# Kernel optimization log

Measured on AMD Instinct MI355X. Metric: run time of the kernel, lower is better.

## Reference

```python
import jax, jax.numpy as jnp
import numpy as np

D_MODEL = 1024
N_HEADS = 16
N_KV = 4
HEAD_DIM = 64
R = 256
B, N = 2, 2048


def setup_inputs() -> dict:
    key = jax.random.key(0)
    ks = jax.random.split(key, 5)
    x = jax.random.normal(ks[0], (B, N, D_MODEL), jnp.float32)
    # rotary cos/sin table: (N, HEAD_DIM//2, 2)
    inv = 1.0 / (10000.0 ** (jnp.arange(0, HEAD_DIM, 2, dtype=jnp.float32) / HEAD_DIM))
    ang = jnp.arange(N, dtype=jnp.float32)[:, None] * inv[None, :]
    freqs_cis = jnp.stack([jnp.cos(ang), jnp.sin(ang)], axis=-1)
    s = 0.02
    Wq = jax.random.normal(ks[1], (D_MODEL, N_HEADS * HEAD_DIM), jnp.float32) * s
    Wk = jax.random.normal(ks[2], (D_MODEL, N_KV * HEAD_DIM), jnp.float32) * s
    Wv = jax.random.normal(ks[3], (D_MODEL, N_KV * HEAD_DIM), jnp.float32) * s
    Wo = jax.random.normal(ks[4], (N_HEADS * HEAD_DIM, D_MODEL), jnp.float32) * s
    return dict(x=x, freqs_cis=freqs_cis, Wq=Wq, Wk=Wk, Wv=Wv, Wo=Wo)


def _select_pairs(scores_i, best_b_i, r):
    """Greedy top-r pair selection with unique-b constraint (one batch row)."""
    half = scores_i.shape[0]
    order = jnp.argsort(-scores_i)  # descending by best similarity

    def step(carry, a_local):
        used, count = carry
        b_local = best_b_i[a_local]
        take = jnp.logical_and(jnp.logical_not(used[b_local]), count < r)
        used = used.at[b_local].set(used[b_local] | take)
        count = count + take.astype(jnp.int32)
        return (used, count), (take, a_local.astype(jnp.int32), b_local.astype(jnp.int32))

    (_, count), (takes, a_locs, b_locs) = jax.lax.scan(
        step, (jnp.zeros(half, bool), jnp.int32(0)), order)
    pos = jnp.cumsum(takes.astype(jnp.int32)) - 1
    idx = jnp.where(takes, pos, r)  # dump non-taken into slot r
    sel_a = jnp.zeros(r + 1, jnp.int32).at[idx].set(a_locs)[:r]
    sel_b = jnp.zeros(r + 1, jnp.int32).at[idx].set(b_locs)[:r]
    valid = jnp.arange(r) < count  # pad (if fewer than r unique) with first pair
    sel_a = jnp.where(valid, sel_a, sel_a[0])
    sel_b = jnp.where(valid, sel_b, sel_b[0])
    return sel_a, sel_b


def bipartite_indices(metric, r):
    """Returns (global_a, global_b, keep_idx) for merge/unmerge."""
    Bm, Nm, _ = metric.shape
    a = metric[:, 0::2]  # (B, half, C)
    b = metric[:, 1::2]
    an = a / jnp.maximum(jnp.linalg.norm(a, axis=-1, keepdims=True), 1e-12)
    bn = b / jnp.maximum(jnp.linalg.norm(b, axis=-1, keepdims=True), 1e-12)
    scores = jnp.einsum('bic,bjc->bij', an, bn)  # (B, half, half)
    best_scores = scores.max(axis=2)
    best_b = scores.argmax(axis=2)
    sel_a, sel_b = jax.vmap(lambda s, m: _select_pairs(s, m, r))(best_scores, best_b)
    global_a = 2 * sel_a      # even indices
    global_b = 2 * sel_b + 1  # odd indices
    bidx = jnp.arange(Bm)[:, None]
    keep_mask = jnp.ones((Bm, Nm), bool).at[bidx, global_b].set(False)
    # stable argsort puts kept (False) positions first, in original order
    keep_idx = jnp.argsort(~keep_mask, axis=1)[:, :Nm - r]
    return global_a, global_b, keep_idx


def merge(x, global_a, global_b, keep_idx):
    Bm = x.shape[0]
    bidx = jnp.arange(Bm)[:, None]
    xa = jnp.take_along_axis(x, global_a[..., None], axis=1)
    xb = jnp.take_along_axis(x, global_b[..., None], axis=1)
    x_out = x.at[bidx, global_a].set((xa + xb) * 0.5)
    return jnp.take_along_axis(x_out, keep_idx[..., None], axis=1)


def unmerge(xm, global_a, global_b, keep_idx, n_orig):
    Bm, _, C = xm.shape
    bidx = jnp.arange(Bm)[:, None]
    out = jnp.zeros((Bm, n_orig, C), xm.dtype).at[bidx, keep_idx].set(xm)
    xa = jnp.take_along_axis(out, global_a[..., None], axis=1)
    return out.at[bidx, global_b].set(xa)


def _rope(t, freqs):
    # t: (B, N, H, HD), freqs: (N, HD//2, 2)
    cos = freqs[None, :, None, :, 0]
    sin = freqs[None, :, None, :, 1]
    t1 = t[..., 0::2]
    t2 = t[..., 1::2]
    rot = jnp.stack([t1 * cos - t2 * sin, t1 * sin + t2 * cos], axis=-1)
    return rot.reshape(t.shape)


def _attention(x_m, freqs, Wq, Wk, Wv, Wo):
    Bm, Nm, _ = x_m.shape
    q = (x_m @ Wq).reshape(Bm, Nm, N_HEADS, HEAD_DIM)
    k = (x_m @ Wk).reshape(Bm, Nm, N_KV, HEAD_DIM)
    v = (x_m @ Wv).reshape(Bm, Nm, N_KV, HEAD_DIM)
    q = _rope(q, freqs)
    k = _rope(k, freqs)
    rep = N_HEADS // N_KV
    k = jnp.repeat(k, rep, axis=2)
    v = jnp.repeat(v, rep, axis=2)
    att = jnp.einsum('bqhd,bkhd->bhqk', q, k) / np.sqrt(HEAD_DIM).astype(np.float32)
    w = jax.nn.softmax(att, axis=-1)
    o = jnp.einsum('bhqk,bkhd->bqhd', w, v).reshape(Bm, Nm, N_HEADS * HEAD_DIM)
    return o @ Wo


def reference(x, freqs_cis, Wq, Wk, Wv, Wo):
    n = x.shape[1]
    metric = jax.lax.stop_gradient(x @ Wk)  # k_proj under no_grad
    ga, gb, ki = bipartite_indices(metric, R)
    x_m = merge(x, ga, gb, ki)
    n_merged = x_m.shape[1]
    out_m = _attention(x_m, freqs_cis[:n_merged], Wq, Wk, Wv, Wo)
    return unmerge(out_m, ga, gb, ki, n)
```

## Files before the change

### kernel.cpp

```cpp
#include <hip/hip_runtime.h>
#include <hip/hip_bf16.h>
#include <math.h>

#define BB 2
#define NN 2048
#define DM 1024
#define NH 16
#define NKV 4
#define HD 64
#define RR 256
#define HALF 1024
#define NM 1792
#define NT 28
#define NSPL 4

typedef __bf16 bf16x8 __attribute__((ext_vector_type(8)));
typedef float f32x4 __attribute__((ext_vector_type(4)));

__device__ inline unsigned pk2(float a, float b) {
  union { __bf16 h; unsigned short u; } ua, ub;
  ua.h = (__bf16)a;
  ub.h = (__bf16)b;
  return (unsigned)ua.u | ((unsigned)ub.u << 16);
}

__device__ inline unsigned shu(unsigned v, int s) {
  return (unsigned)__shfl((int)v, s, 64);
}

__device__ __forceinline__ void async16(const void* g, void* l) {
  __builtin_amdgcn_global_load_lds(
      (const __attribute__((address_space(1))) void*)g,
      (__attribute__((address_space(3))) void*)l, 16, 0, 0);
}

__global__ __launch_bounds__(256) void gemm_bf16(
    const __bf16* __restrict__ A, const __bf16* __restrict__ Bt,
    float* __restrict__ C, int M, int N, int K) {
  __shared__ __align__(16) __bf16 As[8192];
  __shared__ __align__(16) __bf16 Bs[4096];
  const int bm0 = blockIdx.x * 128;
  const int bn0 = blockIdx.y * 64;
  const int w = threadIdx.x >> 6;
  const int lane = threadIdx.x & 63;
  f32x4 acc[2][4];
#pragma unroll
  for (int i = 0; i < 2; ++i)
#pragma unroll
    for (int nt = 0; nt < 4; ++nt) acc[i][nt] = (f32x4){0.f, 0.f, 0.f, 0.f};
  for (int kk = 0; kk < K; kk += 64) {
    __syncthreads();
#pragma unroll
    for (int it = 0; it < 4; ++it) {
      const int c = it * 256 + w * 64 + lane;
      async16(A + (size_t)(bm0 + ((c >> 7) << 4) + (c & 15)) * K + kk +
                  (((c >> 6) & 1) << 5) + (((c >> 4) & 3) << 3),
              &As[(it * 256 + w * 64) * 8]);
    }
#pragma unroll
    for (int it = 0; it < 2; ++it) {
      const int c = it * 256 + w * 64 + lane;
      async16(Bt + (size_t)(bn0 + ((c >> 7) << 4) + (c & 15)) * K + kk +
                  (((c >> 6) & 1) << 5) + (((c >> 4) & 3) << 3),
              &Bs[(it * 256 + w * 64) * 8]);
    }
    __syncthreads();
#pragma unroll
    for (int s = 0; s < 2; ++s) {
      bf16x8 a0 = *(const bf16x8*)&As[((2 * w) * 128 + s * 64 + lane) * 8];
      bf16x8 a1 = *(const bf16x8*)&As[((2 * w + 1) * 128 + s * 64 + lane) * 8];
#pragma unroll
      for (int nt = 0; nt < 4; ++nt) {
        bf16x8 bfr = *(const bf16x8*)&Bs[(nt * 128 + s * 64 + lane) * 8];
        acc[0][nt] =
            __builtin_amdgcn_mfma_f32_16x16x32_bf16(a0, bfr, acc[0][nt], 0, 0, 0);
        acc[1][nt] =
            __builtin_amdgcn_mfma_f32_16x16x32_bf16(a1, bfr, acc[1][nt], 0, 0, 0);
      }
    }
  }
  const int g = lane >> 4, ml = lane & 15;
#pragma unroll
  for (int i = 0; i < 2; ++i)
#pragma unroll
    for (int nt = 0; nt < 4; ++nt)
#pragma unroll
      for (int r = 0; r < 4; ++r)
        C[(size_t)(bm0 + (2 * w + i) * 16 + g * 4 + r) * N + bn0 + nt * 16 +
          ml] = acc[i][nt][r];
}

__global__ __launch_bounds__(256) void gemm_wo(
    const __bf16* __restrict__ A, const __bf16* __restrict__ Bt,
    const int* __restrict__ keep_idx, const int* __restrict__ dst2,
    float* __restrict__ out, int M, int N, int K) {
  __shared__ __align__(16) __bf16 As[8192];
  __shared__ __align__(16) __bf16 Bs[4096];
  const int bm0 = blockIdx.x * 128;
  const int bn0 = blockIdx.y * 64;
  const int w = threadIdx.x >> 6;
  const int lane = threadIdx.x & 63;
  f32x4 acc[2][4];
#pragma unroll
  for (int i = 0; i < 2; ++i)
#pragma unroll
    for (int nt = 0; nt < 4; ++nt) acc[i][nt] = (f32x4){0.f, 0.f, 0.f, 0.f};
  for (int kk = 0; kk < K; kk += 64) {
    __syncthreads();
#pragma unroll
    for (int it = 0; it < 4; ++it) {
      const int c = it * 256 + w * 64 + lane;
      async16(A + (size_t)(bm0 + ((c >> 7) << 4) + (c & 15)) * K + kk +
                  (((c >> 6) & 1) << 5) + (((c >> 4) & 3) << 3),
              &As[(it * 256 + w * 64) * 8]);
    }
#pragma unroll
    for (int it = 0; it < 2; ++it) {
      const int c = it * 256 + w * 64 + lane;
      async16(Bt + (size_t)(bn0 + ((c >> 7) << 4) + (c & 15)) * K + kk +
                  (((c >> 6) & 1) << 5) + (((c >> 4) & 3) << 3),
              &Bs[(it * 256 + w * 64) * 8]);
    }
    __syncthreads();
#pragma unroll
    for (int s = 0; s < 2; ++s) {
      bf16x8 a0 = *(const bf16x8*)&As[((2 * w) * 128 + s * 64 + lane) * 8];
      bf16x8 a1 = *(const bf16x8*)&As[((2 * w + 1) * 128 + s * 64 + lane) * 8];
#pragma unroll
      for (int nt = 0; nt < 4; ++nt) {
        bf16x8 bfr = *(const bf16x8*)&Bs[(nt * 128 + s * 64 + lane) * 8];
        acc[0][nt] =
            __builtin_amdgcn_mfma_f32_16x16x32_bf16(a0, bfr, acc[0][nt], 0, 0, 0);
        acc[1][nt] =
            __builtin_amdgcn_mfma_f32_16x16x32_bf16(a1, bfr, acc[1][nt], 0, 0, 0);
      }
    }
  }
  const int g = lane >> 4, ml = lane & 15;
#pragma unroll
  for (int i = 0; i < 2; ++i)
#pragma unroll
    for (int r = 0; r < 4; ++r) {
      const int row = bm0 + (2 * w + i) * 16 + g * 4 + r;
      const int bb = row / NM, tt = row % NM;
      const int p1 = keep_idx[bb * NM + tt];
      const int p2 = dst2[bb * NM + tt];
#pragma unroll
      for (int nt = 0; nt < 4; ++nt) {
        const int col = bn0 + nt * 16 + ml;
        float v = acc[i][nt][r];
        out[((size_t)(bb * NN + p1)) * DM + col] = v;
        if (p2 >= 0) out[((size_t)(bb * NN + p2)) * DM + col] = v;
      }
    }
}

__global__ __launch_bounds__(256) void gemm3t(
    const __bf16* __restrict__ Ah, const __bf16* __restrict__ Al,
    const __bf16* __restrict__ Bh, const __bf16* __restrict__ Bl,
    float* __restrict__ C0, float* __restrict__ C1, int M, int N, int K) {
  __shared__ __align__(16) __bf16 Ahs[4096], Als[4096], Bhs[4096], Bls[4096];
  const int z = blockIdx.z;
  float* C = z ? C1 : C0;
  const int kof = z * (K / 2);
  const int bm0 = blockIdx.x * 64;
  const int bn0 = blockIdx.y * 64;
  const int w = threadIdx.x >> 6;
  const int lane = threadIdx.x & 63;
  f32x4 acc[4];
#pragma unroll
  for (int nt = 0; nt < 4; ++nt) acc[nt] = (f32x4){0.f, 0.f, 0.f, 0.f};
  for (int kk = kof; kk < kof + K / 2; kk += 64) {
    __syncthreads();
#pragma unroll
    for (int it = 0; it < 2; ++it) {
      const int c = it * 256 + w * 64 + lane;
      const size_t ra = (size_t)(bm0 + ((c >> 7) << 4) + (c & 15)) * K;
      const size_t rb = (size_t)(bn0 + ((c >> 7) << 4) + (c & 15)) * K;
      const int col = kk + (((c >> 6) & 1) << 5) + (((c >> 4) & 3) << 3);
      const int lb = (it * 256 + w * 64) * 8;
      async16(Ah + ra + col, &Ahs[lb]);
      async16(Al + ra + col, &Als[lb]);
      async16(Bh + rb + col, &Bhs[lb]);
      async16(Bl + rb + col, &Bls[lb]);
    }
    __syncthreads();
#pragma unroll
    for (int s = 0; s < 2; ++s) {
      bf16x8 ah = *(const bf16x8*)&Ahs[((w * 2 + s) * 64 + lane) * 8];
      bf16x8 al = *(const bf16x8*)&Als[((w * 2 + s) * 64 + lane) * 8];
#pragma unroll
      for (int nt = 0; nt < 4; ++nt) {
        bf16x8 bh = *(const bf16x8*)&Bhs[((nt * 2 + s) * 64 + lane) * 8];
        bf16x8 bl = *(const bf16x8*)&Bls[((nt * 2 + s) * 64 + lane) * 8];
        acc[nt] = __builtin_amdgcn_mfma_f32_16x16x32_bf16(al, bh, acc[nt], 0, 0, 0);
        acc[nt] = __builtin_amdgcn_mfma_f32_16x16x32_bf16(ah, bl, acc[nt], 0, 0, 0);
        acc[nt] = __builtin_amdgcn_mfma_f32_16x16x32_bf16(ah, bh, acc[nt], 0, 0, 0);
      }
    }
  }
  const int g = lane >> 4, ml = lane & 15;
#pragma unroll
  for (int nt = 0; nt < 4; ++nt)
#pragma unroll
    for (int r = 0; r < 4; ++r)
      C[(size_t)(bm0 + w * 16 + g * 4 + r) * N + bn0 + nt * 16 + ml] =
          acc[nt][r];
}

__global__ __launch_bounds__(256) void gemm_scam(
    const __bf16* __restrict__ Ah, const __bf16* __restrict__ Al,
    const __bf16* __restrict__ Bh, const __bf16* __restrict__ Bl,
    float* __restrict__ sval, int* __restrict__ sidx) {
  __shared__ __align__(16) __bf16 Ahs[4096], Als[4096], Bhs[4096], Bls[4096];
  const size_t zo = (size_t)blockIdx.z * HALF * 256;
  const int bm0 = blockIdx.x * 64;
  const int bn0 = blockIdx.y * 64;
  const int w = threadIdx.x >> 6;
  const int lane = threadIdx.x & 63;
  f32x4 acc[4];
#pragma unroll
  for (int nt = 0; nt < 4; ++nt) acc[nt] = (f32x4){0.f, 0.f, 0.f, 0.f};
  for (int kk = 0; kk < 256; kk += 64) {
    __syncthreads();
#pragma unroll
    for (int it = 0; it < 2; ++it) {
      const int c = it * 256 + w * 64 + lane;
      const size_t ra = zo + (size_t)(bm0 + ((c >> 7) << 4) + (c & 15)) * 256;
      const size_t rb = zo + (size_t)(bn0 + ((c >> 7) << 4) + (c & 15)) * 256;
      const int col = kk + (((c >> 6) & 1) << 5) + (((c >> 4) & 3) << 3);
      const int lb = (it * 256 + w * 64) * 8;
      async16(Ah + ra + col, &Ahs[lb]);
      async16(Al + ra + col, &Als[lb]);
      async16(Bh + rb + col, &Bhs[lb]);
      async16(Bl + rb + col, &Bls[lb]);
    }
    __syncthreads();
#pragma unroll
    for (int s = 0; s < 2; ++s) {
      bf16x8 ah = *(const bf16x8*)&Ahs[((w * 2 + s) * 64 + lane) * 8];
      bf16x8 al = *(const bf16x8*)&Als[((w * 2 + s) * 64 + lane) * 8];
#pragma unroll
      for (int nt = 0; nt < 4; ++nt) {
        bf16x8 bh = *(const bf16x8*)&Bhs[((nt * 2 + s) * 64 + lane) * 8];
        bf16x8 bl = *(const bf16x8*)&Bls[((nt * 2 + s) * 64 + lane) * 8];
        acc[nt] = __builtin_amdgcn_mfma_f32_16x16x32_bf16(al, bh, acc[nt], 0, 0, 0);
        acc[nt] = __builtin_amdgcn_mfma_f32_16x16x32_bf16(ah, bl, acc[nt], 0, 0, 0);
        acc[nt] = __builtin_amdgcn_mfma_f32_16x16x32_bf16(ah, bh, acc[nt], 0, 0, 0);
      }
    }
  }
  const int g = lane >> 4, ml = lane & 15;
#pragma unroll
  for (int r = 0; r < 4; ++r) {
    float bv = acc[0][r];
    int bc = bn0 + ml;
#pragma unroll
    for (int nt = 1; nt < 4; ++nt) {
      float v = acc[nt][r];
      int c = bn0 + nt * 16 + ml;
      if (v > bv) { bv = v; bc = c; }
    }
#pragma unroll
    for (int off = 1; off < 16; off <<= 1) {
      float vo = __shfl_xor(bv, off, 64);
      int co = __shfl_xor(bc, off, 64);
      if (vo > bv || (vo == bv && co < bc)) { bv = vo; bc = co; }
    }
    if (ml == 0) {
      const int row = bm0 + w * 16 + g * 4 + r;
      const size_t o = ((size_t)blockIdx.z * HALF + row) * 16 + (bn0 >> 6);
      sval[o] = bv;
      sidx[o] = bc;
    }
  }
}

__global__ __launch_bounds__(256) void prep_in(
    const float* __restrict__ Wq, const float* __restrict__ Wk,
    const float* __restrict__ Wv, const float* __restrict__ Wo,
    const float* __restrict__ x, __bf16* __restrict__ Wqkvt,
    __bf16* __restrict__ Wktl, __bf16* __restrict__ Wot,
    __bf16* __restrict__ xh, __bf16* __restrict__ xl) {
  const int z = blockIdx.x;
  if (z >= 640) {
    const int i = (z - 640) * 256 + threadIdx.x;
    float4 v = ((const float4*)x)[i];
    float f[4] = {v.x, v.y, v.z, v.w};
    union { __bf16 h[4]; uint2 u; } H, L;
#pragma unroll
    for (int j = 0; j < 4; ++j) {
      __bf16 hh = (__bf16)f[j];
      H.h[j] = hh;
      L.h[j] = (__bf16)(f[j] - (float)hh);
    }
    ((uint2*)xh)[i] = H.u;
    ((uint2*)xl)[i] = L.u;
    return;
  }
  __shared__ float ld[64][65];
  const float* src;
  __bf16* dsth;
  __bf16* dstl = nullptr;
  int N, k0, n0, rowoff;
  if (z < 256) {
    src = Wq; N = 1024; k0 = (z >> 4) << 6; n0 = (z & 15) << 6;
    dsth = Wqkvt; rowoff = 0;
  } else if (z < 320) {
    int zz = z - 256;
    src = Wk; N = 256; k0 = (zz >> 2) << 6; n0 = (zz & 3) << 6;
    dsth = Wqkvt; rowoff = 1024; dstl = Wktl;
  } else if (z < 384) {
    int zz = z - 320;
    src = Wv; N = 256; k0 = (zz >> 2) << 6; n0 = (zz & 3) << 6;
    dsth = Wqkvt; rowoff = 1280;
  } else {
    int zz = z - 384;
    src = Wo; N = 1024; k0 = (zz >> 4) << 6; n0 = (zz & 15) << 6;
    dsth = Wot; rowoff = 0;
  }
  for (int i = threadIdx.x; i < 1024; i += 256) {
    int r = i >> 4, c4 = i & 15;
    float4 v = *(const float4*)(src + (size_t)(k0 + r) * N + n0 + c4 * 4);
    ld[r][c4 * 4 + 0] = v.x;
    ld[r][c4 * 4 + 1] = v.y;
    ld[r][c4 * 4 + 2] = v.z;
    ld[r][c4 * 4 + 3] = v.w;
  }
  __syncthreads();
  for (int i = threadIdx.x; i < 4096; i += 256) {
    int n = i >> 6, k = i & 63;
    float v = ld[k][n];
    __bf16 hh = (__bf16)v;
    dsth[(size_t)(rowoff + n0 + n) * 1024 + k0 + k] = hh;
    if (dstl)
      dstl[(size_t)(n0 + n) * 1024 + k0 + k] = (__bf16)(v - (float)hh);
  }
}

__global__ __launch_bounds__(256) void normalize_split(
    const float* __restrict__ m0, const float* __restrict__ m1,
    __bf16* __restrict__ anh, __bf16* __restrict__ anl,
    __bf16* __restrict__ bnh, __bf16* __restrict__ bnl) {
  const int row = blockIdx.x;
  const int b = row >> 11;
  const int r = row & 2047;
  const int t = threadIdx.x;
  float v = m0[(size_t)row * 256 + t] + m1[(size_t)row * 256 + t];
  float ss = v * v;
#pragma unroll
  for (int o = 32; o > 0; o >>= 1) ss += __shfl_xor(ss, o, 64);
  __shared__ float wsum[4];
  if ((t & 63) == 0) wsum[t >> 6] = ss;
  __syncthreads();
  float tot = wsum[0] + wsum[1] + wsum[2] + wsum[3];
  float inv = 1.f / fmaxf(sqrtf(tot), 1e-12f);
  float nv = v * inv;
  __bf16 hh = (__bf16)nv;
  __bf16 ll = (__bf16)(nv - (float)hh);
  size_t o = ((size_t)b * HALF + (r >> 1)) * 256 + t;
  if (r & 1) {
    bnh[o] = hh;
    bnl[o] = ll;
  } else {
    anh[o] = hh;
    anl[o] = ll;
  }
}

__global__ __launch_bounds__(512) void sort_desc(
    const float* __restrict__ sval, const int* __restrict__ sidx,
    int* __restrict__ best_b, int* __restrict__ order) {
  const int b = blockIdx.x;
  __shared__ float sv[1024];
  __shared__ int si[1024];
  for (int i = threadIdx.x; i < 1024; i += 512) {
    const size_t base = ((size_t)b * HALF + i) * 16;
    float bv = sval[base];
    int bc = sidx[base];
#pragma unroll
    for (int e = 1; e < 16; ++e) {
      float v = sval[base + e];
      int c = sidx[base + e];
      if (v > bv || (v == bv && c < bc)) { bv = v; bc = c; }
    }
    sv[i] = bv;
    si[i] = i;
    best_b[b * HALF + i] = bc;
  }
  __syncthreads();
  for (int k = 2; k <= 1024; k <<= 1) {
    for (int j = k >> 1; j > 0; j >>= 1) {
      for (int t = threadIdx.x; t < 1024; t += 512) {
        int ixj = t ^ j;
        if (ixj > t) {
          bool dir = ((t & k) == 0);
          float va = sv[t], vb = sv[ixj];
          int ia = si[t], ib = si[ixj];
          bool before = (vb > va) || (vb == va && ib < ia);
          if (before == dir) {
            sv[t] = vb; sv[ixj] = va;
            si[t] = ib; si[ixj] = ia;
          }
        }
      }
      __syncthreads();
    }
  }
  for (int i = threadIdx.x; i < 1024; i += 512) order[b * HALF + i] = si[i];
}

__global__ __launch_bounds__(256) void select_and_index(
    const int* __restrict__ best_b, const int* __restrict__ order,
    int* __restrict__ keep_idx, int* __restrict__ partner,
    int* __restrict__ dst2) {
  const int b = blockIdx.x;
  __shared__ int rankA[HALF];
  __shared__ int minrank[HALF];
  __shared__ int taken[HALF];
  __shared__ int sel_a[RR], sel_b[RR];
  __shared__ int removed[NN];
  __shared__ int src_row[NN];
  __shared__ int tsum[256];
  const int t = threadIdx.x;

  for (int i = t; i < HALF; i += 256) { minrank[i] = 0x7fffffff; taken[i] = 0; }
  for (int i = t; i < NN; i += 256) {
    removed[i] = 0;
    partner[b * NN + i] = -1;
  }
  for (int i = t; i < NM; i += 256) dst2[b * NM + i] = -1;
  __syncthreads();
  int ord[4];
#pragma unroll
  for (int q = 0; q < 4; ++q) {
    int step = t * 4 + q;
    ord[q] = order[b * HALF + step];
    rankA[ord[q]] = step;
  }
  __syncthreads();
#pragma unroll
  for (int q = 0; q < 4; ++q) {
    int a = t * 4 + q;
    atomicMin(&minrank[best_b[b * HALF + a]], rankA[a]);
  }
  __syncthreads();
  for (int i = t; i < HALF; i += 256) {
    int mr = minrank[i];
    if (mr != 0x7fffffff) taken[mr] = 1;
  }
  __syncthreads();
  int c[4];
  int mysum = 0;
#pragma unroll
  for (int q = 0; q < 4; ++q) { c[q] = taken[t * 4 + q]; mysum += c[q]; }
  tsum[t] = mysum;
  __syncthreads();
  for (int off = 1; off < 256; off <<= 1) {
    int v = (t >= off) ? tsum[t - off] : 0;
    __syncthreads();
    tsum[t] += v;
    __syncthreads();
  }
  int run = tsum[t] - mysum;
#pragma unroll
  for (int q = 0; q < 4; ++q) {
    if (c[q] && run < RR) {
      int a = ord[q];
      sel_a[run] = 2 * a;
      sel_b[run] = 2 * best_b[b * HALF + a] + 1;
    }
    run += c[q];
  }
  __syncthreads();
  const int cnt = min(tsum[255], RR);
  if (t >= cnt) { sel_a[t] = sel_a[0]; sel_b[t] = sel_b[0]; }
  __syncthreads();
  {
    int ga = sel_a[t], gb = sel_b[t];
    removed[gb] = 1;
    partner[b * NN + ga] = gb;
  }
  __syncthreads();
  int myc = 0;
#pragma unroll
  for (int q = 0; q < 8; ++q) myc += !removed[8 * t + q];
  tsum[t] = myc;
  __syncthreads();
  for (int off = 1; off < 256; off <<= 1) {
    int v = (t >= off) ? tsum[t - off] : 0;
    __syncthreads();
    tsum[t] += v;
    __syncthreads();
  }
  int pos = tsum[t] - myc;
#pragma unroll
  for (int q = 0; q < 8; ++q) {
    int p = 8 * t + q;
    int sr = -1;
    if (!removed[p]) {
      if (pos < NM) {
        keep_idx[b * NM + pos] = p;
        sr = pos;
      }
      ++pos;
    }
    src_row[p] = sr;
  }
  __syncthreads();
  {
    int sr = src_row[sel_a[t]];
    dst2[b * NM + sr] = sel_b[t];
  }
}

__global__ __launch_bounds__(256) void merge_kernel(
    const float* __restrict__ x, const int* __restrict__ keep_idx,
    const int* __restrict__ partner, __bf16* __restrict__ x_mb) {
  const int mrow = blockIdx.x;
  const int b = mrow / NM;
  const int t = mrow % NM;
  const int p = keep_idx[b * NM + t];
  const int pp = partner[b * NN + p];
  const float4* src =
      reinterpret_cast<const float4*>(x + ((size_t)b * NN + p) * DM);
  float4 val = src[threadIdx.x];
  if (pp >= 0) {
    const float4* s2 =
        reinterpret_cast<const float4*>(x + ((size_t)b * NN + pp) * DM);
    float4 v2 = s2[threadIdx.x];
    val.x = 0.5f * (val.x + v2.x);
    val.y = 0.5f * (val.y + v2.y);
    val.z = 0.5f * (val.z + v2.z);
    val.w = 0.5f * (val.w + v2.w);
  }
  union { __bf16 h[4]; uint2 u; } U;
  U.h[0] = (__bf16)val.x;
  U.h[1] = (__bf16)val.y;
  U.h[2] = (__bf16)val.z;
  U.h[3] = (__bf16)val.w;
  ((uint2*)(x_mb + (size_t)mrow * DM))[threadIdx.x] = U.u;
}

__global__ __launch_bounds__(256) void prep_qkv(
    const float* __restrict__ qkv, const float* __restrict__ fc,
    __bf16* __restrict__ qbh, __bf16* __restrict__ kbh,
    __bf16* __restrict__ vtb) {
  __shared__ float ld[64][65];
  const int z = blockIdx.x;
  if (z < BB * NM) {
    const int row = z;
    const int t = row % NM;
    const int b = row / NM;
    for (int idx = threadIdx.x; idx < 640; idx += 256) {
      int u = idx & 31;
      float c = fc[(t * 32 + u) * 2];
      float s = fc[(t * 32 + u) * 2 + 1];
      if (idx < 512) {
        int h = idx >> 5;
        const float* p = qkv + (size_t)row * 1536 + h * 64 + 2 * u;
        float x1 = p[0], x2 = p[1];
        __bf16* d = qbh + ((size_t)(b * NH + h) * NM + t) * 64 + 2 * u;
        d[0] = (__bf16)((x1 * c - x2 * s) * 0.125f);
        d[1] = (__bf16)((x1 * s + x2 * c) * 0.125f);
      } else {
        int h = (idx - 512) >> 5;
        const float* p = qkv + (size_t)row * 1536 + 1024 + h * 64 + 2 * u;
        float x1 = p[0], x2 = p[1];
        __bf16* d = kbh + ((size_t)(b * NKV + h) * NM + t) * 64 + 2 * u;
        d[0] = (__bf16)(x1 * c - x2 * s);
        d[1] = (__bf16)(x1 * s + x2 * c);
      }
    }
    return;
  }
  int bid = z - BB * NM;
  const int kt = bid % (NM / 64); bid /= (NM / 64);
  const int kvh = bid % NKV;
  const int b = bid / NKV;
  const int j0 = kt * 64;
  for (int t2 = threadIdx.x; t2 < 1024; t2 += 256) {
    int key = t2 >> 4, c4 = t2 & 15;
    float4 v4 = *reinterpret_cast<const float4*>(
        qkv + (size_t)(b * NM + j0 + key) * 1536 + 1280 + kvh * 64 + c4 * 4);
    ld[key][c4 * 4 + 0] = v4.x;
    ld[key][c4 * 4 + 1] = v4.y;
    ld[key][c4 * 4 + 2] = v4.z;
    ld[key][c4 * 4 + 3] = v4.w;
  }
  __syncthreads();
  const int dim = threadIdx.x >> 2, kc = threadIdx.x & 3;
  __bf16* out = vtb + ((size_t)(b * NKV + kvh) * 64 + dim) * NM + j0 + kc * 16;
#pragma unroll
  for (int kk = 0; kk < 16; ++kk) out[kk] = (__bf16)ld[kc * 16 + kk][dim];
}

__global__ __launch_bounds__(512) void attn_mfma(
    const __bf16* __restrict__ qbh, const __bf16* __restrict__ kbh,
    const __bf16* __restrict__ vtb, float* __restrict__ pl,
    __bf16* __restrict__ pacc) {
  __shared__ __align__(16) __bf16 Ks[2][4096];
  __shared__ __align__(16) __bf16 Vs[2][4096];
  int bid = blockIdx.x;
  const int qt2 = bid % (NM / 32); bid /= (NM / 32);
  const int split = bid % NSPL; bid /= NSPL;
  const int kvh = bid % NKV;
  const int b = bid / NKV;
  const int w = threadIdx.x >> 6;
  const int lane = threadIdx.x & 63;
  const int h = kvh * 4 + (w & 3);
  const int qt = qt2 * 32 + (w >> 2) * 16;
  const int g = lane >> 4;
  const int ml = lane & 15;

  const __bf16* qrow = qbh + ((size_t)(b * NH + h) * NM + qt + ml) * 64;
  bf16x8 qa0 = *reinterpret_cast<const bf16x8*>(qrow + g * 8);
  bf16x8 qa1 = *reinterpret_cast<const bf16x8*>(qrow + 32 + g * 8);

  f32x4 acc[4];
#pragma unroll
  for (int mt = 0; mt < 4; ++mt) acc[mt] = (f32x4){0.f, 0.f, 0.f, 0.f};
  float lsum = 0.f;

  const __bf16* kp = kbh + (size_t)(b * NKV + kvh) * NM * 64;
  const __bf16* vp = vtb + (size_t)(b * NKV + kvh) * 64 * NM;
  const int src0 = ((lane >> 4) & 1) * 32 + ml;
  const int src1 = src0 + 16;
  const int sel = g >> 1;
  const int c = threadIdx.x;
  const int lb = w * 512;
  const size_t koff = (size_t)(((c >> 7) << 4) + (c & 15)) * 64 +
                      (((c >> 6) & 1) << 5) + (((c >> 4) & 3) << 3);
  const size_t voff = (size_t)(((c >> 7) << 4) + (c & 15)) * NM +
                      (((c >> 6) & 1) << 5) + (((c >> 4) & 3) << 3);

  const int jt0 = split * (NT / NSPL);
  const int niter = NT / NSPL;
  async16(kp + (size_t)jt0 * 64 * 64 + koff, &Ks[0][lb]);
  async16(vp + jt0 * 64 + voff, &Vs[0][lb]);

  for (int i = 0; i < niter; ++i) {
    __syncthreads();
    if (i + 1 < niter) {
      const int jn = jt0 + i + 1;
      async16(kp + (size_t)jn * 64 * 64 + koff, &Ks[(i + 1) & 1][lb]);
      async16(vp + jn * 64 + voff, &Vs[(i + 1) & 1][lb]);
    }
    const __bf16* Kb = Ks[i & 1];
    const __bf16* Vb = Vs[i & 1];
    f32x4 S[4];
#pragma unroll
    for (int nt = 0; nt < 4; ++nt) {
      bf16x8 k0 = *(const bf16x8*)&Kb[(nt * 128 + lane) * 8];
      bf16x8 k1 = *(const bf16x8*)&Kb[(nt * 128 + 64 + lane) * 8];
      f32x4 s4 = (f32x4){0.f, 0.f, 0.f, 0.f};
      s4 = __builtin_amdgcn_mfma_f32_16x16x32_bf16(k0, qa0, s4, 0, 0, 0);
      s4 = __builtin_amdgcn_mfma_f32_16x16x32_bf16(k1, qa1, s4, 0, 0, 0);
      S[nt] = s4;
    }
    float p[4][4];
#pragma unroll
    for (int nt = 0; nt < 4; ++nt)
#pragma unroll
      for (int r = 0; r < 4; ++r) {
        p[nt][r] = __expf(S[nt][r]);
        lsum += p[nt][r];
      }
    unsigned pk[4][2];
#pragma unroll
    for (int nt = 0; nt < 4; ++nt) {
      pk[nt][0] = pk2(p[nt][0], p[nt][1]);
      pk[nt][1] = pk2(p[nt][2], p[nt][3]);
    }
    unsigned A00 = shu(pk[0][0], src0), A01 = shu(pk[0][1], src0);
    unsigned A10 = shu(pk[1][0], src0), A11 = shu(pk[1][1], src0);
    unsigned B00 = shu(pk[0][0], src1), B01 = shu(pk[0][1], src1);
    unsigned B10 = shu(pk[1][0], src1), B11 = shu(pk[1][1], src1);
    unsigned C00 = shu(pk[2][0], src0), C01 = shu(pk[2][1], src0);
    unsigned C10 = shu(pk[3][0], src0), C11 = shu(pk[3][1], src0);
    unsigned D00 = shu(pk[2][0], src1), D01 = shu(pk[2][1], src1);
    unsigned D10 = shu(pk[3][0], src1), D11 = shu(pk[3][1], src1);
    union { uint4 u; bf16x8 v; } P0, P1;
    P0.u.x = sel ? A10 : A00; P0.u.y = sel ? A11 : A01;
    P0.u.z = sel ? B10 : B00; P0.u.w = sel ? B11 : B01;
    P1.u.x = sel ? C10 : C00; P1.u.y = sel ? C11 : C01;
    P1.u.z = sel ? D10 : D00; P1.u.w = sel ? D11 : D01;
#pragma unroll
    for (int mt = 0; mt < 4; ++mt) {
      bf16x8 v0 = *(const bf16x8*)&Vb[(mt * 128 + lane) * 8];
      bf16x8 v1 = *(const bf16x8*)&Vb[(mt * 128 + 64 + lane) * 8];
      acc[mt] = __builtin_amdgcn_mfma_f32_16x16x32_bf16(v0, P0.v, acc[mt], 0, 0, 0);
      acc[mt] = __builtin_amdgcn_mfma_f32_16x16x32_bf16(v1, P1.v, acc[mt], 0, 0, 0);
    }
  }
  lsum += __shfl_xor(lsum, 16, 64);
  lsum += __shfl_xor(lsum, 32, 64);
  const size_t row = (size_t)(b * NH + h) * NM + qt + ml;
  if (g == 0) pl[row * NSPL + split] = lsum;
  __bf16* pa = pacc + (row * NSPL + split) * 64;
#pragma unroll
  for (int mt = 0; mt < 4; ++mt) {
    uint2 u;
    u.x = pk2(acc[mt][0], acc[mt][1]);
    u.y = pk2(acc[mt][2], acc[mt][3]);
    *reinterpret_cast<uint2*>(pa + mt * 16 + g * 4) = u;
  }
}

__global__ __launch_bounds__(256) void attn_combine(
    const float* __restrict__ pl, const __bf16* __restrict__ pacc,
    __bf16* __restrict__ attn_ob) {
  const size_t rid = (size_t)blockIdx.x * 4 + (threadIdx.x >> 6);
  const int d = threadIdx.x & 63;
  float num = 0.f, den = 0.f;
#pragma unroll
  for (int s = 0; s < NSPL; ++s) {
    num += (float)pacc[(rid * NSPL + s) * 64 + d];
    den += pl[rid * NSPL + s];
  }
  float o = num / den;
  const int q = (int)(rid % NM);
  const int h = (int)((rid / NM) % NH);
  const int b = (int)(rid / ((size_t)NM * NH));
  attn_ob[((size_t)(b * NM + q)) * DM + h * 64 + d] = (__bf16)o;
}

extern "C" void kernel_launch(void* const* d_in, const int* in_sizes, int n_in,
                              void* d_out, int out_size, void* d_ws,
                              size_t ws_size, hipStream_t stream) {
  const float* x = (const float*)d_in[0];
  const float* fc = (const float*)d_in[1];
  const float* Wq = (const float*)d_in[2];
  const float* Wk = (const float*)d_in[3];
  const float* Wv = (const float*)d_in[4];
  const float* Wo = (const float*)d_in[5];
  float* out = (float*)d_out;

  char* ws = (char*)d_ws;
  size_t off = 0;
  auto alloc = [&](size_t bytes) {
    void* p = ws + off;
    off += (bytes + 255) & ~(size_t)255;
    return p;
  };
  float* metric0 = (float*)alloc((size_t)BB * NN * 256 * 4);
  float* metric1 = (float*)alloc((size_t)BB * NN * 256 * 4);
  int* best_b = (int*)alloc((size_t)BB * HALF * 4);
  int* order = (int*)alloc((size_t)BB * HALF * 4);
  int* keep_idx = (int*)alloc((size_t)BB * NM * 4);
  int* partner = (int*)alloc((size_t)BB * NN * 4);
  int* dst2 = (int*)alloc((size_t)BB * NM * 4);
  float* sval = (float*)alloc((size_t)BB * HALF * 16 * 4);
  int* sidx = (int*)alloc((size_t)BB * HALF * 16 * 4);
  char* bigreg = (char*)alloc((size_t)30 * 1024 * 1024);
  __bf16* xh = (__bf16*)bigreg;
  __bf16* xl = (__bf16*)(bigreg + (size_t)8704 * 1024);
  __bf16* anh = (__bf16*)bigreg;
  __bf16* anl = (__bf16*)(bigreg + (size_t)1100 * 1024);
  __bf16* bnh = (__bf16*)(bigreg + (size_t)2200 * 1024);
  __bf16* bnl = (__bf16*)(bigreg + (size_t)3300 * 1024);
  float* qkv = (float*)bigreg;
  __bf16* pacc = (__bf16*)bigreg;
  __bf16* x_mb = (__bf16*)alloc((size_t)BB * NM * DM * 2);
  __bf16* qbh = (__bf16*)alloc((size_t)BB * NH * NM * 64 * 2);
  __bf16* kbh = (__bf16*)alloc((size_t)BB * NKV * NM * 64 * 2);
  __bf16* vtb = (__bf16*)alloc((size_t)BB * NKV * 64 * NM * 2);
  __bf16* attn_ob = (__bf16*)alloc((size_t)BB * NM * DM * 2);
  float* pl = (float*)alloc((size_t)BB * NH * NM * NSPL * 4);
  __bf16* Wqkvt = (__bf16*)alloc((size_t)1536 * DM * 2);
  __bf16* Wktl = (__bf16*)alloc((size_t)256 * DM * 2);
  __bf16* Wot = (__bf16*)alloc((size_t)DM * DM * 2);
  const __bf16* Wkth = Wqkvt + (size_t)1024 * 1024;

  prep_in<<<640 + (BB * NN * DM / 4) / 256, 256, 0, stream>>>(
      Wq, Wk, Wv, Wo, x, Wqkvt, Wktl, Wot, xh, xl);
  gemm3t<<<dim3(64, 4, 2), 256, 0, stream>>>(xh, xl, Wkth, Wktl, metric0,
                                             metric1, BB * NN, 256, DM);
  normalize_split<<<BB * NN, 256, 0, stream>>>(metric0, metric1, anh, anl, bnh,
                                               bnl);
  gemm_scam<<<dim3(16, 16, 2), 256, 0, stream>>>(anh, anl, bnh, bnl, sval,
                                                 sidx);
  sort_desc<<<BB, 512, 0, stream>>>(sval, sidx, best_b, order);
  select_and_index<<<BB, 256, 0, stream>>>(best_b, order, keep_idx, partner,
                                           dst2);
  merge_kernel<<<BB * NM, 256, 0, stream>>>(x, keep_idx, partner, x_mb);
  gemm_bf16<<<dim3(28, 24), 256, 0, stream>>>(x_mb, Wqkvt, qkv, BB * NM, 1536,
                                              DM);
  prep_qkv<<<BB * NM + BB * NKV * (NM / 64), 256, 0, stream>>>(qkv, fc, qbh,
                                                               kbh, vtb);
  attn_mfma<<<BB * NKV * NSPL * (NM / 32), 512, 0, stream>>>(qbh, kbh, vtb, pl,
                                                             pacc);
  attn_combine<<<(BB * NH * NM) / 4, 256, 0, stream>>>(pl, pacc, attn_ob);
  gemm_wo<<<dim3(28, 16), 256, 0, stream>>>(attn_ob, Wot, keep_idx, dst2, out,
                                            BB * NM, DM, DM);
}
```

Measured before the change: 291.6 us.

## Shrink attention blocks to 256 threads and drop K/V double buffering

The attention kernel now uses 4 waves per block, each covering one head of the KV group for a 16-row query tile, instead of 8 waves covering two query tiles. The double-buffered async K/V prefetch is replaced by a single buffer that is loaded and then synchronised before use every iteration. This halves shared memory per block and doubles the block count, aiming for higher occupancy. In exchange, load latency is no longer overlapped with MFMA work, and K/V tiles are fetched twice as often in total because each tile is shared by fewer query rows.

```diff
diff --git a/kernel.cpp b/kernel.cpp
--- a/kernel.cpp
+++ b/kernel.cpp
@@ -595,21 +595,21 @@
   for (int kk = 0; kk < 16; ++kk) out[kk] = (__bf16)ld[kc * 16 + kk][dim];
 }
 
-__global__ __launch_bounds__(512) void attn_mfma(
+__global__ __launch_bounds__(256) void attn_mfma(
     const __bf16* __restrict__ qbh, const __bf16* __restrict__ kbh,
     const __bf16* __restrict__ vtb, float* __restrict__ pl,
     __bf16* __restrict__ pacc) {
-  __shared__ __align__(16) __bf16 Ks[2][4096];
-  __shared__ __align__(16) __bf16 Vs[2][4096];
+  __shared__ __align__(16) __bf16 Ks[4096];
+  __shared__ __align__(16) __bf16 Vs[4096];
   int bid = blockIdx.x;
-  const int qt2 = bid % (NM / 32); bid /= (NM / 32);
+  const int qt1 = bid % (NM / 16); bid /= (NM / 16);
   const int split = bid % NSPL; bid /= NSPL;
   const int kvh = bid % NKV;
   const int b = bid / NKV;
   const int w = threadIdx.x >> 6;
   const int lane = threadIdx.x & 63;
-  const int h = kvh * 4 + (w & 3);
-  const int qt = qt2 * 32 + (w >> 2) * 16;
+  const int h = kvh * 4 + w;
+  const int qt = qt1 * 16;
   const int g = lane >> 4;
   const int ml = lane & 15;
 
@@ -627,32 +627,27 @@
   const int src0 = ((lane >> 4) & 1) * 32 + ml;
   const int src1 = src0 + 16;
   const int sel = g >> 1;
-  const int c = threadIdx.x;
-  const int lb = w * 512;
-  const size_t koff = (size_t)(((c >> 7) << 4) + (c & 15)) * 64 +
-                      (((c >> 6) & 1) << 5) + (((c >> 4) & 3) << 3);
-  const size_t voff = (size_t)(((c >> 7) << 4) + (c & 15)) * NM +
-                      (((c >> 6) & 1) << 5) + (((c >> 4) & 3) << 3);
 
   const int jt0 = split * (NT / NSPL);
-  const int niter = NT / NSPL;
-  async16(kp + (size_t)jt0 * 64 * 64 + koff, &Ks[0][lb]);
-  async16(vp + jt0 * 64 + voff, &Vs[0][lb]);
-
-  for (int i = 0; i < niter; ++i) {
-    __syncthreads();
-    if (i + 1 < niter) {
-      const int jn = jt0 + i + 1;
-      async16(kp + (size_t)jn * 64 * 64 + koff, &Ks[(i + 1) & 1][lb]);
-      async16(vp + jn * 64 + voff, &Vs[(i + 1) & 1][lb]);
-    }
-    const __bf16* Kb = Ks[i & 1];
-    const __bf16* Vb = Vs[i & 1];
+  for (int jt = jt0; jt < jt0 + NT / NSPL; ++jt) {
+    __syncthreads();
+#pragma unroll
+    for (int it = 0; it < 2; ++it) {
+      const int c = it * 256 + w * 64 + lane;
+      const int lb = (it * 256 + w * 64) * 8;
+      async16(kp + (size_t)(jt * 64 + ((c >> 7) << 4) + (c & 15)) * 64 +
+                  (((c >> 6) & 1) << 5) + (((c >> 4) & 3) << 3),
+              &Ks[lb]);
+      async16(vp + (size_t)(((c >> 7) << 4) + (c & 15)) * NM + jt * 64 +
+                  (((c >> 6) & 1) << 5) + (((c >> 4) & 3) << 3),
+              &Vs[lb]);
+    }
+    __syncthreads();
     f32x4 S[4];
 #pragma unroll
     for (int nt = 0; nt < 4; ++nt) {
-      bf16x8 k0 = *(const bf16x8*)&Kb[(nt * 128 + lane) * 8];
-      bf16x8 k1 = *(const bf16x8*)&Kb[(nt * 128 + 64 + lane) * 8];
+      bf16x8 k0 = *(const bf16x8*)&Ks[(nt * 128 + lane) * 8];
+      bf16x8 k1 = *(const bf16x8*)&Ks[(nt * 128 + 64 + lane) * 8];
       f32x4 s4 = (f32x4){0.f, 0.f, 0.f, 0.f};
       s4 = __builtin_amdgcn_mfma_f32_16x16x32_bf16(k0, qa0, s4, 0, 0, 0);
       s4 = __builtin_amdgcn_mfma_f32_16x16x32_bf16(k1, qa1, s4, 0, 0, 0);
@@ -687,8 +682,8 @@
     P1.u.z = sel ? D10 : D00; P1.u.w = sel ? D11 : D01;
 #pragma unroll
     for (int mt = 0; mt < 4; ++mt) {
-      bf16x8 v0 = *(const bf16x8*)&Vb[(mt * 128 + lane) * 8];
-      bf16x8 v1 = *(const bf16x8*)&Vb[(mt * 128 + 64 + lane) * 8];
+      bf16x8 v0 = *(const bf16x8*)&Vs[(mt * 128 + lane) * 8];
+      bf16x8 v1 = *(const bf16x8*)&Vs[(mt * 128 + 64 + lane) * 8];
       acc[mt] = __builtin_amdgcn_mfma_f32_16x16x32_bf16(v0, P0.v, acc[mt], 0, 0, 0);
       acc[mt] = __builtin_amdgcn_mfma_f32_16x16x32_bf16(v1, P1.v, acc[mt], 0, 0, 0);
     }
@@ -788,7 +783,7 @@
                                               DM);
   prep_qkv<<<BB * NM + BB * NKV * (NM / 64), 256, 0, stream>>>(qkv, fc, qbh,
                                                                kbh, vtb);
-  attn_mfma<<<BB * NKV * NSPL * (NM / 32), 512, 0, stream>>>(qbh, kbh, vtb, pl,
+  attn_mfma<<<BB * NKV * NSPL * (NM / 16), 256, 0, stream>>>(qbh, kbh, vtb, pl,
                                                              pacc);
   attn_combine<<<(BB * NH * NM) / 4, 256, 0, stream>>>(pl, pacc, attn_ob);
   gemm_wo<<<dim3(28, 16), 256, 0, stream>>>(attn_ob, Wot, keep_idx, dst2, out,
```

Measured after the change: 300.9 us. +3.2%, slower.
